# Kernel tuning notes

Measured on AMD Instinct MI355X. Metric: run time of the kernel, lower is better.

Reference implementation:

```python
import jax, jax.numpy as jnp
import numpy as np

B, S, D_IN, D_OUT = 4, 4096, 1024, 1024

def setup_inputs() -> dict:
    key = jax.random.key(0)
    kx, kq, kk, kv = jax.random.split(key, 4)
    scale = 1.0 / np.sqrt(D_IN)
    return {
        "x": jax.random.normal(kx, (B, S, D_IN), dtype=jnp.float32),
        "Wq": jax.random.normal(kq, (D_IN, D_OUT), dtype=jnp.float32) * scale,
        "Wk": jax.random.normal(kk, (D_IN, D_OUT), dtype=jnp.float32) * scale,
        "Wv": jax.random.normal(kv, (D_IN, D_OUT), dtype=jnp.float32) * scale,
    }

def reference(x, Wq, Wk, Wv):
    # x: [B, S, d_in]; W*: [d_in, d_out]
    B_, S_, _ = x.shape
    d_out = Wq.shape[1]
    q = jnp.einsum("bsi,io->bso", x, Wq)
    k = jnp.einsum("bsi,io->bso", x, Wk)
    v = jnp.einsum("bsi,io->bso", x, Wv)
    # scores: [B, S, S]
    scores = jnp.einsum("bqo,bko->bqk", q, k)
    # causal mask: position q attends to k <= q (intended semantics of the
    # tril-buffer masked_fill); masked entries -> -inf before softmax.
    causal = jnp.tril(jnp.ones((S_, S_), dtype=bool))  # True where allowed
    scores = jnp.where(causal[None, :, :], scores, -jnp.inf)
    attn = jax.nn.softmax(scores / jnp.sqrt(jnp.asarray(d_out, scores.dtype)), axis=-1)
    # dropout p=0.0 -> identity
    return jnp.einsum("bqk,bko->bqo", attn, v)
```

## Files before the change

kernel.cpp:

```cpp
#include <hip/hip_runtime.h>


typedef __attribute__((ext_vector_type(8))) short bh8;
typedef __attribute__((ext_vector_type(4))) float f32x4;
typedef __attribute__((ext_vector_type(4))) unsigned int u32x4;
typedef __attribute__((ext_vector_type(2))) unsigned int u32x2;

#define BATCH 4
#define SEQ   4096
#define DIM   1024
#define MTOT  (BATCH * SEQ)

__device__ __forceinline__ unsigned short f2bf(float f) {
  union { float f; unsigned int u; } v; v.f = f;
  return (unsigned short)((v.u + 0x7FFFu + ((v.u >> 16) & 1u)) >> 16);
}

__global__ __launch_bounds__(256)
void k_convert_x(const float* __restrict__ x, unsigned short* __restrict__ xb) {
  size_t idx = ((size_t)blockIdx.x * 256 + threadIdx.x) * 8;
  f32x4 v0 = *(const f32x4*)(x + idx);
  f32x4 v1 = *(const f32x4*)(x + idx + 4);
  u32x4 pk;
  pk[0] = (unsigned)f2bf(v0[0]) | ((unsigned)f2bf(v0[1]) << 16);
  pk[1] = (unsigned)f2bf(v0[2]) | ((unsigned)f2bf(v0[3]) << 16);
  pk[2] = (unsigned)f2bf(v1[0]) | ((unsigned)f2bf(v1[1]) << 16);
  pk[3] = (unsigned)f2bf(v1[2]) | ((unsigned)f2bf(v1[3]) << 16);
  *(u32x4*)(xb + idx) = pk;
}

__global__ __launch_bounds__(256)
void k_transpose_w(const float* __restrict__ Wq, const float* __restrict__ Wk,
                   const float* __restrict__ Wv, unsigned short* __restrict__ wt) {
  __shared__ float tile[32][33];
  const int z = blockIdx.z;
  const float* W = (z == 0) ? Wq : ((z == 1) ? Wk : Wv);
  unsigned short* out = wt + (size_t)z * DIM * DIM;
  const int tx = threadIdx.x, ty = threadIdx.y;
  const int n = blockIdx.x * 32 + tx;
  const int k = blockIdx.y * 32 + ty;
#pragma unroll
  for (int i = 0; i < 32; i += 8)
    tile[ty + i][tx] = W[(size_t)(k + i) * DIM + n];
  __syncthreads();
  const int k2 = blockIdx.y * 32 + tx;
  const int n2 = blockIdx.x * 32 + ty;
#pragma unroll
  for (int i = 0; i < 32; i += 8)
    out[(size_t)(n2 + i) * DIM + k2] = f2bf(tile[tx][ty + i]);
}

__global__ __launch_bounds__(256)
void k_qkv_gemm(const unsigned short* __restrict__ xb, const unsigned short* __restrict__ wt,
                unsigned short* __restrict__ qb, unsigned short* __restrict__ kb,
                unsigned short* __restrict__ vt) {
  const int tid = threadIdx.x;
  const int l = tid & 63, w = tid >> 6;
  const int lane16 = l & 15, quad = l >> 4;
  const int wm = w & 1, wn = w >> 1;
  const int m0 = blockIdx.x * 128, n0 = blockIdx.y * 128, z = blockIdx.z;
  const unsigned short* wtz = wt + (size_t)z * DIM * DIM;

  __shared__ unsigned short As[128][40];
  __shared__ unsigned short Bs[128][40];

  f32x4 acc[4][4];
#pragma unroll
  for (int i = 0; i < 4; ++i)
#pragma unroll
    for (int j = 0; j < 4; ++j) acc[i][j] = (f32x4){0.f, 0.f, 0.f, 0.f};

  for (int k0 = 0; k0 < DIM; k0 += 32) {
#pragma unroll
    for (int i = 0; i < 2; ++i) {
      int c = tid + i * 256;
      int row = c >> 2, cc = (c & 3) * 8;
      *(bh8*)&As[row][cc] = *(const bh8*)(xb  + (size_t)(m0 + row) * DIM + k0 + cc);
      *(bh8*)&Bs[row][cc] = *(const bh8*)(wtz + (size_t)(n0 + row) * DIM + k0 + cc);
    }
    __syncthreads();
    bh8 a[4], b[4];
#pragma unroll
    for (int mt = 0; mt < 4; ++mt) a[mt] = *(const bh8*)&As[wm * 64 + mt * 16 + lane16][quad * 8];
#pragma unroll
    for (int nt = 0; nt < 4; ++nt) b[nt] = *(const bh8*)&Bs[wn * 64 + nt * 16 + lane16][quad * 8];
#pragma unroll
    for (int mt = 0; mt < 4; ++mt)
#pragma unroll
      for (int nt = 0; nt < 4; ++nt)
        acc[mt][nt] = __builtin_amdgcn_mfma_f32_16x16x32_bf16(a[mt], b[nt], acc[mt][nt], 0, 0, 0);
    __syncthreads();
  }

  if (z < 2) {
    unsigned short* outp = (z == 0) ? qb : kb;
#pragma unroll
    for (int mt = 0; mt < 4; ++mt)
#pragma unroll
      for (int nt = 0; nt < 4; ++nt) {
        int row = m0 + wm * 64 + mt * 16 + quad * 4;
        int col = n0 + wn * 64 + nt * 16 + lane16;
#pragma unroll
        for (int r = 0; r < 4; ++r)
          outp[(size_t)(row + r) * DIM + col] = f2bf(acc[mt][nt][r]);
      }
  } else {
#pragma unroll
    for (int mt = 0; mt < 4; ++mt)
#pragma unroll
      for (int nt = 0; nt < 4; ++nt) {
        int m = m0 + wm * 64 + mt * 16 + quad * 4;
        int bb = m >> 12, s = m & (SEQ - 1);
        int col = n0 + wn * 64 + nt * 16 + lane16;
        unsigned long long pk =
            (unsigned long long)f2bf(acc[mt][nt][0]) |
            ((unsigned long long)f2bf(acc[mt][nt][1]) << 16) |
            ((unsigned long long)f2bf(acc[mt][nt][2]) << 32) |
            ((unsigned long long)f2bf(acc[mt][nt][3]) << 48);
        *(unsigned long long*)(vt + (size_t)bb * DIM * SEQ + (size_t)col * SEQ + s) = pk;
      }
  }
}

__global__ __launch_bounds__(512, 2)
void k_attn(const unsigned short* __restrict__ qb, const unsigned short* __restrict__ kb,
            const unsigned short* __restrict__ vt, float* __restrict__ out) {
  const int tid = threadIdx.x;
  const int w = tid >> 6;
  const int l = tid & 63;
  const int lane16 = l & 15, quad = l >> 4;
  const int batch = blockIdx.x;
  const int pid = blockIdx.y;

  __shared__ float Pp[8][32][68];
  __shared__ unsigned short Psh[32][72];
  __shared__ float row_m[32], row_l[32], row_alpha[32];

  const size_t bbase = (size_t)batch * SEQ;
  const unsigned short* vtb = vt + (size_t)batch * DIM * SEQ;
  const float cexp = 0.04508422002778f;

  for (int half = 0; half < 2; ++half) {
    const int t = (half == 0) ? pid : (127 - pid);
    const int q0 = t * 32;

    bh8 qf[2][4];
#pragma unroll
    for (int mt = 0; mt < 2; ++mt)
#pragma unroll
      for (int c = 0; c < 4; ++c)
        qf[mt][c] = *(const bh8*)(qb + (bbase + q0 + mt * 16 + lane16) * DIM +
                                  w * 128 + c * 32 + quad * 8);

    f32x4 o[2][8];
#pragma unroll
    for (int mt = 0; mt < 2; ++mt)
#pragma unroll
      for (int nt = 0; nt < 8; ++nt) o[mt][nt] = (f32x4){0.f, 0.f, 0.f, 0.f};

    const int nk = (q0 + 95) >> 6;

    bh8 kf[4][4];
#pragma unroll
    for (int kt = 0; kt < 4; ++kt)
#pragma unroll
      for (int c = 0; c < 4; ++c)
        kf[kt][c] = *(const bh8*)(kb + (bbase + kt * 16 + lane16) * DIM +
                                  w * 128 + c * 32 + quad * 8);

    for (int it = 0; it < nk; ++it) {
      const int k0 = it * 64;

      bh8 vfa[4][2];
#pragma unroll
      for (int nt = 0; nt < 4; ++nt)
#pragma unroll
        for (int kc = 0; kc < 2; ++kc)
          vfa[nt][kc] = *(const bh8*)(vtb + (size_t)(w * 128 + nt * 16 + lane16) * SEQ +
                                      k0 + kc * 32 + quad * 8);

      if (it == 0 && tid < 32) { row_m[tid] = -3.0e38f; row_l[tid] = 0.f; }

#pragma unroll
      for (int kt = 0; kt < 4; ++kt) {
        if (k0 + kt * 16 <= q0 + 31) {
#pragma unroll
          for (int mt = 0; mt < 2; ++mt) {
            f32x4 s = (f32x4){0.f, 0.f, 0.f, 0.f};
#pragma unroll
            for (int c = 0; c < 4; ++c)
              s = __builtin_amdgcn_mfma_f32_16x16x32_bf16(qf[mt][c], kf[kt][c], s, 0, 0, 0);
            int row = mt * 16 + quad * 4;
            int col = kt * 16 + lane16;
#pragma unroll
            for (int r = 0; r < 4; ++r)
              Pp[w][row + r][col] = s[r];
          }
        }
      }

      if (it + 1 < nk) {
#pragma unroll
        for (int kt = 0; kt < 4; ++kt)
#pragma unroll
          for (int c = 0; c < 4; ++c)
            kf[kt][c] = *(const bh8*)(kb + (bbase + k0 + 64 + kt * 16 + lane16) * DIM +
                                      w * 128 + c * 32 + quad * 8);
      }
      __syncthreads();

      {
        int r = tid >> 4, c0 = (tid & 15) * 4;
        int q = q0 + r;
        f32x4 sv = *(const f32x4*)&Pp[0][r][c0];
#pragma unroll
        for (int ww = 1; ww < 8; ++ww)
          sv += *(const f32x4*)&Pp[ww][r][c0];
#pragma unroll
        for (int j = 0; j < 4; ++j)
          if (k0 + c0 + j > q) sv[j] = -3.0e38f;
        float mx = fmaxf(fmaxf(sv[0], sv[1]), fmaxf(sv[2], sv[3]));
#pragma unroll
        for (int off = 1; off < 16; off <<= 1)
          mx = fmaxf(mx, __shfl_xor(mx, off));
        float mold = row_m[r];
        float mnew = fmaxf(mold, mx);
        float p0 = __builtin_amdgcn_exp2f((sv[0] - mnew) * cexp);
        float p1 = __builtin_amdgcn_exp2f((sv[1] - mnew) * cexp);
        float p2 = __builtin_amdgcn_exp2f((sv[2] - mnew) * cexp);
        float p3 = __builtin_amdgcn_exp2f((sv[3] - mnew) * cexp);
        float sum = (p0 + p1) + (p2 + p3);
#pragma unroll
        for (int off = 1; off < 16; off <<= 1)
          sum += __shfl_xor(sum, off);
        float alpha = __builtin_amdgcn_exp2f((mold - mnew) * cexp);
        u32x2 pk;
        pk[0] = (unsigned)f2bf(p0) | ((unsigned)f2bf(p1) << 16);
        pk[1] = (unsigned)f2bf(p2) | ((unsigned)f2bf(p3) << 16);
        *(u32x2*)&Psh[r][c0] = pk;
        if ((tid & 15) == 0) {
          row_m[r] = mnew;
          row_l[r] = alpha * row_l[r] + sum;
          row_alpha[r] = alpha;
        }
      }
      __syncthreads();

      {
        bh8 vfb[4][2];
#pragma unroll
        for (int nt = 0; nt < 4; ++nt)
#pragma unroll
          for (int kc = 0; kc < 2; ++kc)
            vfb[nt][kc] = *(const bh8*)(vtb + (size_t)(w * 128 + (nt + 4) * 16 + lane16) * SEQ +
                                        k0 + kc * 32 + quad * 8);

#pragma unroll
        for (int mt = 0; mt < 2; ++mt) {
          f32x4 al;
#pragma unroll
          for (int r = 0; r < 4; ++r) al[r] = row_alpha[mt * 16 + quad * 4 + r];
#pragma unroll
          for (int nt = 0; nt < 8; ++nt) o[mt][nt] *= al;
        }
        bh8 pf[2][2];
#pragma unroll
        for (int mt = 0; mt < 2; ++mt)
#pragma unroll
          for (int kc = 0; kc < 2; ++kc)
            pf[mt][kc] = *(const bh8*)&Psh[mt * 16 + lane16][kc * 32 + quad * 8];
#pragma unroll
        for (int kc = 0; kc < 2; ++kc) {
          if (k0 + kc * 32 <= q0 + 31) {
#pragma unroll
            for (int nt = 0; nt < 4; ++nt)
#pragma unroll
              for (int mt = 0; mt < 2; ++mt)
                o[mt][nt] = __builtin_amdgcn_mfma_f32_16x16x32_bf16(pf[mt][kc], vfa[nt][kc], o[mt][nt], 0, 0, 0);
#pragma unroll
            for (int nt = 0; nt < 4; ++nt)
#pragma unroll
              for (int mt = 0; mt < 2; ++mt)
                o[mt][nt + 4] = __builtin_amdgcn_mfma_f32_16x16x32_bf16(pf[mt][kc], vfb[nt][kc], o[mt][nt + 4], 0, 0, 0);
          }
        }
      }
    }

#pragma unroll
    for (int mt = 0; mt < 2; ++mt) {
      int row = mt * 16 + quad * 4;
      float il[4];
#pragma unroll
      for (int r = 0; r < 4; ++r) il[r] = 1.0f / row_l[row + r];
#pragma unroll
      for (int nt = 0; nt < 8; ++nt) {
        size_t base = (bbase + q0 + row) * DIM + w * 128 + nt * 16 + lane16;
#pragma unroll
        for (int r = 0; r < 4; ++r)
          out[base + (size_t)r * DIM] = o[mt][nt][r] * il[r];
      }
    }
    __syncthreads();
  }
}

extern "C" void kernel_launch(void* const* d_in, const int* in_sizes, int n_in,
                              void* d_out, int out_size, void* d_ws, size_t ws_size,
                              hipStream_t stream) {
  const float* x  = (const float*)d_in[0];
  const float* Wq = (const float*)d_in[1];
  const float* Wk = (const float*)d_in[2];
  const float* Wv = (const float*)d_in[3];
  float* out = (float*)d_out;

  char* ws = (char*)d_ws;
  const size_t XB_BYTES = (size_t)MTOT * DIM * 2;
  const size_t WT_BYTES = (size_t)3 * DIM * DIM * 2;
  unsigned short* xb = (unsigned short*)(ws);
  unsigned short* wt = (unsigned short*)(ws + XB_BYTES);
  unsigned short* qb = (unsigned short*)(ws + XB_BYTES + WT_BYTES);
  unsigned short* kb = qb + (size_t)MTOT * DIM;
  unsigned short* vt = kb + (size_t)MTOT * DIM;

  k_convert_x<<<dim3((MTOT * DIM) / (256 * 8)), dim3(256), 0, stream>>>(x, xb);
  k_transpose_w<<<dim3(32, 32, 3), dim3(32, 8), 0, stream>>>(Wq, Wk, Wv, wt);
  k_qkv_gemm<<<dim3(MTOT / 128, DIM / 128, 3), dim3(256), 0, stream>>>(xb, wt, qb, kb, vt);
  k_attn<<<dim3(BATCH, 64), dim3(512), 0, stream>>>(qb, kb, vt, out);
}
```

Measured before the change: 901.6 us.

## Prefetch V fragments one iteration ahead and relax barriers in attention loop

Loads of both V fragment halves move out of the current iteration and are issued for the next key block right after the PV MFMAs, so global latency overlaps the next QK and softmax phases. __syncthreads is replaced with a barrier that only waits on LDS counters (lgkmcnt), which lets outstanding global prefetches stay in flight across barriers. s_setprio is raised around MFMA sections to favour matrix work across waves. Register pressure grows because vfa and vfb are now live across the whole loop.

```diff
diff --git a/kernel.cpp b/kernel.cpp
--- a/kernel.cpp
+++ b/kernel.cpp
@@ -15,6 +15,13 @@
   union { float f; unsigned int u; } v; v.f = f;
   return (unsigned short)((v.u + 0x7FFFu + ((v.u >> 16) & 1u)) >> 16);
 }
+
+#define BAR()                                                \
+  do {                                                       \
+    asm volatile("s_waitcnt lgkmcnt(0)" ::: "memory");       \
+    __builtin_amdgcn_s_barrier();                            \
+    asm volatile("" ::: "memory");                           \
+  } while (0)
 
 __global__ __launch_bounds__(256)
 void k_convert_x(const float* __restrict__ x, unsigned short* __restrict__ xb) {
@@ -167,20 +174,23 @@
       for (int c = 0; c < 4; ++c)
         kf[kt][c] = *(const bh8*)(kb + (bbase + kt * 16 + lane16) * DIM +
                                   w * 128 + c * 32 + quad * 8);
+    bh8 vfa[4][2], vfb[4][2];
+#pragma unroll
+    for (int nt = 0; nt < 4; ++nt)
+#pragma unroll
+      for (int kc = 0; kc < 2; ++kc) {
+        vfa[nt][kc] = *(const bh8*)(vtb + (size_t)(w * 128 + nt * 16 + lane16) * SEQ +
+                                    kc * 32 + quad * 8);
+        vfb[nt][kc] = *(const bh8*)(vtb + (size_t)(w * 128 + (nt + 4) * 16 + lane16) * SEQ +
+                                    kc * 32 + quad * 8);
+      }
+
+    if (tid < 32) { row_m[tid] = -3.0e38f; row_l[tid] = 0.f; }
 
     for (int it = 0; it < nk; ++it) {
       const int k0 = it * 64;
 
-      bh8 vfa[4][2];
-#pragma unroll
-      for (int nt = 0; nt < 4; ++nt)
-#pragma unroll
-        for (int kc = 0; kc < 2; ++kc)
-          vfa[nt][kc] = *(const bh8*)(vtb + (size_t)(w * 128 + nt * 16 + lane16) * SEQ +
-                                      k0 + kc * 32 + quad * 8);
-
-      if (it == 0 && tid < 32) { row_m[tid] = -3.0e38f; row_l[tid] = 0.f; }
-
+      __builtin_amdgcn_s_setprio(1);
 #pragma unroll
       for (int kt = 0; kt < 4; ++kt) {
         if (k0 + kt * 16 <= q0 + 31) {
@@ -198,6 +208,7 @@
           }
         }
       }
+      __builtin_amdgcn_s_setprio(0);
 
       if (it + 1 < nk) {
 #pragma unroll
@@ -207,7 +218,7 @@
             kf[kt][c] = *(const bh8*)(kb + (bbase + k0 + 64 + kt * 16 + lane16) * DIM +
                                       w * 128 + c * 32 + quad * 8);
       }
-      __syncthreads();
+      BAR();
 
       {
         int r = tid >> 4, c0 = (tid & 15) * 4;
@@ -244,17 +255,9 @@
           row_alpha[r] = alpha;
         }
       }
-      __syncthreads();
+      BAR();
 
       {
-        bh8 vfb[4][2];
-#pragma unroll
-        for (int nt = 0; nt < 4; ++nt)
-#pragma unroll
-          for (int kc = 0; kc < 2; ++kc)
-            vfb[nt][kc] = *(const bh8*)(vtb + (size_t)(w * 128 + (nt + 4) * 16 + lane16) * SEQ +
-                                        k0 + kc * 32 + quad * 8);
-
 #pragma unroll
         for (int mt = 0; mt < 2; ++mt) {
           f32x4 al;
@@ -269,6 +272,7 @@
 #pragma unroll
           for (int kc = 0; kc < 2; ++kc)
             pf[mt][kc] = *(const bh8*)&Psh[mt * 16 + lane16][kc * 32 + quad * 8];
+        __builtin_amdgcn_s_setprio(1);
 #pragma unroll
         for (int kc = 0; kc < 2; ++kc) {
           if (k0 + kc * 32 <= q0 + 31) {
@@ -284,6 +288,19 @@
                 o[mt][nt + 4] = __builtin_amdgcn_mfma_f32_16x16x32_bf16(pf[mt][kc], vfb[nt][kc], o[mt][nt + 4], 0, 0, 0);
           }
         }
+        __builtin_amdgcn_s_setprio(0);
+
+        if (it + 1 < nk) {
+#pragma unroll
+          for (int nt = 0; nt < 4; ++nt)
+#pragma unroll
+            for (int kc = 0; kc < 2; ++kc) {
+              vfa[nt][kc] = *(const bh8*)(vtb + (size_t)(w * 128 + nt * 16 + lane16) * SEQ +
+                                          k0 + 64 + kc * 32 + quad * 8);
+              vfb[nt][kc] = *(const bh8*)(vtb + (size_t)(w * 128 + (nt + 4) * 16 + lane16) * SEQ +
+                                          k0 + 64 + kc * 32 + quad * 8);
+            }
+        }
       }
     }
 
@@ -301,7 +318,7 @@
           out[base + (size_t)r * DIM] = o[mt][nt][r] * il[r];
       }
     }
-    __syncthreads();
+    BAR();
   }
 }
 
```

Measured after the change: 1.120 ms. 1.24x slower.
